# Kernel tuning notes

Hardware: AMD Instinct MI355X
Metric: run time of the kernel (lower is better)

## Reference

```python
import jax, jax.numpy as jnp
import numpy as np

FRAME_LENGTH = 1024
FRAME_STEP = 256
FFT_LENGTH = 1024
NUM_FRAMES = 8192


def setup_inputs() -> dict:
    key = jax.random.key(0)
    k1, k2 = jax.random.split(key)
    S_real = jax.random.normal(k1, (NUM_FRAMES, FFT_LENGTH), dtype=jnp.float32)
    S_imag = jax.random.normal(k2, (NUM_FRAMES, FFT_LENGTH), dtype=jnp.float32)
    return {"S_real": S_real, "S_imag": S_imag}


def reference(S_real, S_imag):
    num_frames, F = S_real.shape
    n = jnp.float32(F)
    two_pi = jnp.float32(2.0 * np.pi)
    k = jnp.arange(F, dtype=jnp.float32)
    theta = two_pi * k / n                      # [F]
    c, s = jnp.cos(theta), jnp.sin(theta)
    # degenerate per-bin 'IDFT' rotation, exactly as in the original math:
    # real_ifft = (real*c - imag*s)/n ; imag_ifft = (real*s + imag*c)/n
    # time_frame = real_ifft - imag_ifft
    time_frames = ((S_real - S_imag) * c - (S_real + S_imag) * s) / n  # [N, F]
    # periodic Hann window
    window = 0.5 - 0.5 * jnp.cos(two_pi * jnp.arange(FRAME_LENGTH, dtype=jnp.float32) / FRAME_LENGTH)
    frames = time_frames * window               # [N, F]
    out_len = FRAME_STEP * (num_frames - 1) + FRAME_LENGTH
    # overlap-add indices: idx[i, j] = i*step + j
    idx = (jnp.arange(num_frames)[:, None] * FRAME_STEP
           + jnp.arange(FRAME_LENGTH)[None, :]).reshape(-1)
    output_signal = jnp.zeros(out_len, dtype=jnp.float32).at[idx].add(frames.reshape(-1))
    window_correction = jnp.zeros(out_len, dtype=jnp.float32).at[idx].add(
        jnp.broadcast_to(window, (num_frames, FRAME_LENGTH)).reshape(-1))
    return output_signal / jnp.maximum(window_correction, 1e-8)
```

## Files before the change

kernel.cpp:

```cpp
#include <hip/hip_runtime.h>
#include <math.h>

#define FFT_LEN   1024
#define STEP      256
#define NFRAMES   8192
#define OUT_LEN   (STEP * (NFRAMES - 1) + FFT_LEN)
#define NVEC      (OUT_LEN / 4)

__global__ __launch_bounds__(256) void istft_ola_kernel(
    const float* __restrict__ Sr,
    const float* __restrict__ Si,
    float* __restrict__ out)
{
    __shared__ float As[FFT_LEN];
    __shared__ float Bs[FFT_LEN];
    __shared__ float Ws[FFT_LEN];

    const float inv_n  = 1.0f / 1024.0f;
    const float two_pi = 6.283185307179586f;

    for (int j = (int)threadIdx.x; j < FFT_LEN; j += 256) {
        float theta = two_pi * (float)j * inv_n;
        float s, c;
        sincosf(theta, &s, &c);
        float w = 0.5f - 0.5f * c;
        As[j] = (c - s) * w * inv_n;
        Bs[j] = (c + s) * w * inv_n;
        Ws[j] = w;
    }
    __syncthreads();

    int v = (int)blockIdx.x * 256 + (int)threadIdx.x;
    if (v >= NVEC) return;

    int t0 = v << 2;
    int m0 = t0 & (STEP - 1);
    int q  = t0 >> 8;

    float4 num = make_float4(0.f, 0.f, 0.f, 0.f);
    float4 den = make_float4(0.f, 0.f, 0.f, 0.f);

#pragma unroll
    for (int a = 0; a < 4; ++a) {
        int i = q - a;
        if ((unsigned)i < (unsigned)NFRAMES) {
            int j = m0 + a * STEP;
            size_t base = (size_t)i * FFT_LEN + (size_t)j;
            const float4 R = *reinterpret_cast<const float4*>(Sr + base);
            const float4 I = *reinterpret_cast<const float4*>(Si + base);
            const float4 A = *reinterpret_cast<const float4*>(&As[j]);
            const float4 B = *reinterpret_cast<const float4*>(&Bs[j]);
            const float4 W = *reinterpret_cast<const float4*>(&Ws[j]);
            num.x = fmaf(R.x, A.x, fmaf(-I.x, B.x, num.x));
            num.y = fmaf(R.y, A.y, fmaf(-I.y, B.y, num.y));
            num.z = fmaf(R.z, A.z, fmaf(-I.z, B.z, num.z));
            num.w = fmaf(R.w, A.w, fmaf(-I.w, B.w, num.w));
            den.x += W.x; den.y += W.y; den.z += W.z; den.w += W.w;
        }
    }

    float4 o;
    o.x = num.x / fmaxf(den.x, 1e-8f);
    o.y = num.y / fmaxf(den.y, 1e-8f);
    o.z = num.z / fmaxf(den.z, 1e-8f);
    o.w = num.w / fmaxf(den.w, 1e-8f);
    *reinterpret_cast<float4*>(out + t0) = o;
}

extern "C" void kernel_launch(void* const* d_in, const int* in_sizes, int n_in,
                              void* d_out, int out_size, void* d_ws, size_t ws_size,
                              hipStream_t stream) {
    const float* Sr = (const float*)d_in[0];
    const float* Si = (const float*)d_in[1];
    float* out = (float*)d_out;
    (void)in_sizes; (void)n_in; (void)out_size; (void)d_ws; (void)ws_size;

    dim3 block(256);
    dim3 grid((NVEC + 255) / 256);
    istft_ola_kernel<<<grid, block, 0, stream>>>(Sr, Si, out);
}
```

Before: 92.26 us.

## Compute twiddles in registers, use constant window sum, process two vectors per thread

Replaces the shared-memory twiddle tables and their barrier with per-thread sincos of four angles, deriving the other three quarter-period twiddles by symmetry. Interior outputs use the fact that the Hann window overlap sum with step 256 is the constant 2, so they multiply by 0.5 instead of dividing. Each thread now handles two output vectors with a fixed grid of 1025 blocks, which amortizes the sincos setup. The kernel is memory-bound on reading 64MB, so any gain is likely small; the constant window sum introduces minor rounding differences.

```diff
diff --git a/kernel.cpp b/kernel.cpp
--- a/kernel.cpp
+++ b/kernel.cpp
@@ -6,65 +6,96 @@
 #define NFRAMES   8192
 #define OUT_LEN   (STEP * (NFRAMES - 1) + FFT_LEN)
 #define NVEC      (OUT_LEN / 4)
+#define NBLK      1025
+#define VSTRIDE   (NBLK * 256)
 
 __global__ __launch_bounds__(256) void istft_ola_kernel(
     const float* __restrict__ Sr,
     const float* __restrict__ Si,
     float* __restrict__ out)
 {
-    __shared__ float As[FFT_LEN];
-    __shared__ float Bs[FFT_LEN];
-    __shared__ float Ws[FFT_LEN];
-
     const float inv_n  = 1.0f / 1024.0f;
     const float two_pi = 6.283185307179586f;
 
-    for (int j = (int)threadIdx.x; j < FFT_LEN; j += 256) {
-        float theta = two_pi * (float)j * inv_n;
-        float s, c;
-        sincosf(theta, &s, &c);
-        float w = 0.5f - 0.5f * c;
-        As[j] = (c - s) * w * inv_n;
-        Bs[j] = (c + s) * w * inv_n;
-        Ws[j] = w;
+    const int v0 = (int)blockIdx.x * 256 + (int)threadIdx.x;
+    const int m0 = (v0 << 2) & (STEP - 1);
+
+    float c[4], s[4];
+#pragma unroll
+    for (int d = 0; d < 4; ++d) {
+        float theta = two_pi * (float)(m0 + d) * inv_n;
+        sincosf(theta, &s[d], &c[d]);
     }
-    __syncthreads();
 
-    int v = (int)blockIdx.x * 256 + (int)threadIdx.x;
-    if (v >= NVEC) return;
-
-    int t0 = v << 2;
-    int m0 = t0 & (STEP - 1);
-    int q  = t0 >> 8;
-
-    float4 num = make_float4(0.f, 0.f, 0.f, 0.f);
-    float4 den = make_float4(0.f, 0.f, 0.f, 0.f);
-
+    float A[4][4], B[4][4], W[4][4];
 #pragma unroll
-    for (int a = 0; a < 4; ++a) {
-        int i = q - a;
-        if ((unsigned)i < (unsigned)NFRAMES) {
-            int j = m0 + a * STEP;
-            size_t base = (size_t)i * FFT_LEN + (size_t)j;
-            const float4 R = *reinterpret_cast<const float4*>(Sr + base);
-            const float4 I = *reinterpret_cast<const float4*>(Si + base);
-            const float4 A = *reinterpret_cast<const float4*>(&As[j]);
-            const float4 B = *reinterpret_cast<const float4*>(&Bs[j]);
-            const float4 W = *reinterpret_cast<const float4*>(&Ws[j]);
-            num.x = fmaf(R.x, A.x, fmaf(-I.x, B.x, num.x));
-            num.y = fmaf(R.y, A.y, fmaf(-I.y, B.y, num.y));
-            num.z = fmaf(R.z, A.z, fmaf(-I.z, B.z, num.z));
-            num.w = fmaf(R.w, A.w, fmaf(-I.w, B.w, num.w));
-            den.x += W.x; den.y += W.y; den.z += W.z; den.w += W.w;
+    for (int d = 0; d < 4; ++d) {
+        const float cc = c[d], ss = s[d];
+#pragma unroll
+        for (int a = 0; a < 4; ++a) {
+            const float ca = (a == 0) ? cc : (a == 1) ? -ss : (a == 2) ? -cc : ss;
+            const float sa = (a == 0) ? ss : (a == 1) ? cc  : (a == 2) ? -ss : -cc;
+            const float w  = 0.5f - 0.5f * ca;
+            A[a][d] = (ca - sa) * w * inv_n;
+            B[a][d] = (ca + sa) * w * inv_n;
+            W[a][d] = w;
         }
     }
 
-    float4 o;
-    o.x = num.x / fmaxf(den.x, 1e-8f);
-    o.y = num.y / fmaxf(den.y, 1e-8f);
-    o.z = num.z / fmaxf(den.z, 1e-8f);
-    o.w = num.w / fmaxf(den.w, 1e-8f);
-    *reinterpret_cast<float4*>(out + t0) = o;
+#pragma unroll
+    for (int half = 0; half < 2; ++half) {
+        const int v = v0 + half * VSTRIDE;
+        if (half == 1 && v >= NVEC) break;
+
+        const int t0 = v << 2;
+        const int q  = t0 >> 8;
+
+        float num[4] = {0.f, 0.f, 0.f, 0.f};
+
+        if (q >= 3 && q <= NFRAMES - 1) {
+#pragma unroll
+            for (int a = 0; a < 4; ++a) {
+                const size_t base = (size_t)(q - a) * FFT_LEN + (size_t)(m0 + a * STEP);
+                const float4 R = *reinterpret_cast<const float4*>(Sr + base);
+                const float4 I = *reinterpret_cast<const float4*>(Si + base);
+                num[0] = fmaf(R.x, A[a][0], fmaf(-I.x, B[a][0], num[0]));
+                num[1] = fmaf(R.y, A[a][1], fmaf(-I.y, B[a][1], num[1]));
+                num[2] = fmaf(R.z, A[a][2], fmaf(-I.z, B[a][2], num[2]));
+                num[3] = fmaf(R.w, A[a][3], fmaf(-I.w, B[a][3], num[3]));
+            }
+            float4 o;
+            o.x = num[0] * 0.5f;
+            o.y = num[1] * 0.5f;
+            o.z = num[2] * 0.5f;
+            o.w = num[3] * 0.5f;
+            *reinterpret_cast<float4*>(out + t0) = o;
+        } else {
+            float den[4] = {0.f, 0.f, 0.f, 0.f};
+#pragma unroll
+            for (int a = 0; a < 4; ++a) {
+                const int i = q - a;
+                if ((unsigned)i < (unsigned)NFRAMES) {
+                    const size_t base = (size_t)i * FFT_LEN + (size_t)(m0 + a * STEP);
+                    const float4 R = *reinterpret_cast<const float4*>(Sr + base);
+                    const float4 I = *reinterpret_cast<const float4*>(Si + base);
+                    num[0] = fmaf(R.x, A[a][0], fmaf(-I.x, B[a][0], num[0]));
+                    num[1] = fmaf(R.y, A[a][1], fmaf(-I.y, B[a][1], num[1]));
+                    num[2] = fmaf(R.z, A[a][2], fmaf(-I.z, B[a][2], num[2]));
+                    num[3] = fmaf(R.w, A[a][3], fmaf(-I.w, B[a][3], num[3]));
+                    den[0] += W[a][0];
+                    den[1] += W[a][1];
+                    den[2] += W[a][2];
+                    den[3] += W[a][3];
+                }
+            }
+            float4 o;
+            o.x = num[0] / fmaxf(den[0], 1e-8f);
+            o.y = num[1] / fmaxf(den[1], 1e-8f);
+            o.z = num[2] / fmaxf(den[2], 1e-8f);
+            o.w = num[3] / fmaxf(den[3], 1e-8f);
+            *reinterpret_cast<float4*>(out + t0) = o;
+        }
+    }
 }
 
 extern "C" void kernel_launch(void* const* d_in, const int* in_sizes, int n_in,
@@ -76,6 +107,6 @@
     (void)in_sizes; (void)n_in; (void)out_size; (void)d_ws; (void)ws_size;
 
     dim3 block(256);
-    dim3 grid((NVEC + 255) / 256);
+    dim3 grid(NBLK);
     istft_ola_kernel<<<grid, block, 0, stream>>>(Sr, Si, out);
 }
```

Result: no change. 92.22 us, median of 2 (-0.0%).
